# Optimization experiments

Hardware: AMD Instinct MI355X
Metric: run time of the kernel (lower is better)

## Reference

```python
import jax, jax.numpy as jnp
import numpy as np
import math

DIM = 1024
MAX_DEPTH = 16
ROPE_BASE = 10000.0
NUM_ACTIVE = 2

def setup_inputs() -> dict:
    key = jax.random.key(0)
    ks = jax.random.split(key, 6)
    bsz, seq, dim, E, hidden = 4, 1024, DIM, 8, 4 * DIM
    bound = 1.0 / math.sqrt(dim)
    return {
        "x": jax.random.normal(ks[0], (bsz, seq, dim), jnp.float32),
        "router_w": jax.random.normal(ks[1], (dim, dim), jnp.float32) * 0.02,
        "expert_keys": jax.random.uniform(ks[2], (E, dim), jnp.float32, -bound, bound),
        "expert_bias": jnp.zeros((E,), jnp.float32),
        "fc_w": jax.random.normal(ks[3], (E, hidden, dim), jnp.float32) * 0.02,
        "proj_w": jax.random.normal(ks[4], (E, dim, hidden), jnp.float32) * 0.02,
        "depth_idx": 3,
    }

def _rope_row(depth_idx, rev_idx, dtype):
    half = DIM // 2
    inv_freq = 1.0 / (ROPE_BASE ** (jnp.arange(0, DIM, 2, dtype=jnp.float32) / DIM))  # [half]
    f = depth_idx * inv_freq
    r = rev_idx * inv_freq
    return (jnp.cos(f).astype(dtype), jnp.sin(f).astype(dtype),
            jnp.cos(r).astype(dtype), jnp.sin(r).astype(dtype))

def reference(x, router_w, expert_keys, expert_bias, fc_w, proj_w, depth_idx):
    bsz, seq, dim = x.shape
    N = bsz * seq
    flat_x = x.reshape(N, dim)
    # router + RMSNorm (no weight, eps = machine eps, matching F.rms_norm default)
    q = flat_x @ router_w.T
    eps = jnp.asarray(jnp.finfo(q.dtype).eps, q.dtype)
    q = q * jax.lax.rsqrt(jnp.mean(q * q, axis=-1, keepdims=True) + eps)
    # depth RoPE (forward freq on first half pairing, reverse freq on second half)
    half = dim // 2
    cos, sin, rcos, rsin = _rope_row(float(depth_idx), float(MAX_DEPTH - 1 - depth_idx), q.dtype)
    q1, q2 = q[..., :half], q[..., half:]
    q = jnp.concatenate((q1 * cos + q2 * sin, -q1 * rsin + q2 * rcos), axis=-1)
    # routing
    logits = (q @ expert_keys.T) / math.sqrt(dim)  # [N, E]
    gate_values = jax.nn.sigmoid(logits)
    biased = logits + expert_bias
    _, topk_idx = jax.lax.top_k(biased, NUM_ACTIVE)  # [N, k]
    topk_gates = jnp.take_along_axis(gate_values, topk_idx, axis=-1)
    topk_gates = topk_gates / jnp.clip(topk_gates.sum(-1, keepdims=True), 1e-9, None)
    gates = jnp.zeros_like(gate_values).at[jnp.arange(N)[:, None], topk_idx].set(topk_gates)
    # dense all-expert MLP: relu(x W_fc^T)^2 W_proj^T, then mask-and-sum
    h = jax.nn.relu(jnp.einsum('nd,ehd->neh', flat_x, fc_w))
    expert_out = jnp.einsum('neh,edh->ned', h * h, proj_w)  # [N, E, dim]
    y = jnp.einsum('ned,ne->nd', expert_out, gates)
    return y.reshape(bsz, seq, dim)
```

## Files before the change

kernel.cpp:

```cpp
#include <hip/hip_runtime.h>
#include <hip/hip_bf16.h>
#include <math.h>

#define N_TOK 4096
#define DIM_V 1024
#define NEXP  8
#define HID   4096
#define NSLOT 9216

typedef short  s16x8 __attribute__((ext_vector_type(8)));
typedef unsigned short u16x8 __attribute__((ext_vector_type(8)));
typedef float  f32x4 __attribute__((ext_vector_type(4)));

constexpr size_t OFF_XB   = 0;
constexpr size_t OFF_WB   = OFF_XB + 8388608;
constexpr size_t OFF_RK   = OFF_WB + 2097152;
constexpr size_t OFF_KPP  = OFF_RK + 65536;
constexpr size_t OFF_SSQ  = OFF_KPP + 65536;
constexpr size_t OFF_CNT  = OFF_SSQ + 16384;
constexpr size_t OFF_CUR  = OFF_CNT + 128;
constexpr size_t OFF_TOK  = OFF_CUR + 128;
constexpr size_t OFF_GSL  = OFF_TOK + 36864;
constexpr size_t ZERO_BEG = OFF_KPP;
constexpr size_t ZERO_END = OFF_GSL + 36864;
constexpr size_t OFF_OFFP = ZERO_END;
constexpr size_t OFF_IDX2 = OFF_OFFP + 128;
constexpr size_t OFF_G2   = OFF_IDX2 + 32768;
constexpr size_t OFF_INV  = OFF_G2 + 32768;
constexpr size_t SMALL_END = OFF_INV + 32768;

constexpr size_t A_OFF_FCB = SMALL_END;
constexpr size_t A_OFF_PO  = A_OFF_FCB;
constexpr size_t A_OFF_PJB = A_OFF_FCB + 67108864;
constexpr size_t A_OFF_H2  = A_OFF_PJB + 67108864;
constexpr size_t WS_FULL   = A_OFF_H2 + 75497472;

__device__ inline unsigned short f2bf(float f) {
  __hip_bfloat16 h = __float2bfloat16(f);
  return __builtin_bit_cast(unsigned short, h);
}

__device__ __forceinline__ void gload16(const void* g, void* l) {
  __builtin_amdgcn_global_load_lds(
      (const __attribute__((address_space(1))) unsigned int*)g,
      (__attribute__((address_space(3))) unsigned int*)l, 16, 0, 0);
}

__global__ __launch_bounds__(256) void k_cvt_all(
    const float* __restrict__ x, const float* __restrict__ rw,
    const float* __restrict__ fw, const float* __restrict__ pw,
    unsigned short* __restrict__ xb, unsigned short* __restrict__ wb,
    unsigned short* __restrict__ fcb, unsigned short* __restrict__ pjb) {
  constexpr int NX4 = (N_TOK * DIM_V) / 4;
  constexpr int NW4 = (DIM_V * DIM_V) / 4;
  constexpr int NF4 = (NEXP * HID * DIM_V) / 4;
  constexpr int NU  = (NX4 + NW4 + 2 * NF4) / 1024;
  const int upb = (NU + (int)gridDim.x - 1) / (int)gridDim.x;
  for (int k = 0; k < upb; ++k) {
    int u = (int)blockIdx.x * upb + k;
    if (u >= NU) break;
    int f4 = u * 1024;
    const float4* s; unsigned short* d; int base;
    if (f4 < NX4)                   { s = (const float4*)x;  d = xb;  base = f4; }
    else if (f4 < NX4 + NW4)        { s = (const float4*)rw; d = wb;  base = f4 - NX4; }
    else if (f4 < NX4 + NW4 + NF4)  { s = (const float4*)fw; d = fcb; base = f4 - NX4 - NW4; }
    else                            { s = (const float4*)pw; d = pjb; base = f4 - NX4 - NW4 - NF4; }
    int j = base + (int)threadIdx.x;
    float4 v0 = s[j];
    float4 v1 = s[j + 256];
    float4 v2 = s[j + 512];
    float4 v3 = s[j + 768];
    ushort4 o0 = { f2bf(v0.x), f2bf(v0.y), f2bf(v0.z), f2bf(v0.w) };
    ushort4 o1 = { f2bf(v1.x), f2bf(v1.y), f2bf(v1.z), f2bf(v1.w) };
    ushort4 o2 = { f2bf(v2.x), f2bf(v2.y), f2bf(v2.z), f2bf(v2.w) };
    ushort4 o3 = { f2bf(v3.x), f2bf(v3.y), f2bf(v3.z), f2bf(v3.w) };
    *(ushort4*)(d + (size_t)j * 4)           = o0;
    *(ushort4*)(d + (size_t)(j + 256) * 4)   = o1;
    *(ushort4*)(d + (size_t)(j + 512) * 4)   = o2;
    *(ushort4*)(d + (size_t)(j + 768) * 4)   = o3;
  }
}

__global__ void k_ropekeys(const float* __restrict__ keys, const int* __restrict__ depth,
                           double* __restrict__ rk) {
  int i = threadIdx.x;
  if (i >= 512) return;
  int dep = depth[0];
  double p = pow(10000.0, (double)i / 512.0);
  float invf = 1.0f / (float)p;
  float ff = (float)dep * invf;
  float rr = (float)(15 - dep) * invf;
  float cf  = (float)cos((double)ff);
  float sf  = (float)sin((double)ff);
  float rcf = (float)cos((double)rr);
  float rsf = (float)sin((double)rr);
  for (int e = 0; e < NEXP; ++e) {
    double k1 = (double)keys[e * DIM_V + i];
    double k2 = (double)keys[e * DIM_V + 512 + i];
    rk[e * DIM_V + i]       = (double)cf  * k1 - (double)rsf * k2;
    rk[e * DIM_V + 512 + i] = (double)sf  * k1 + (double)rcf * k2;
  }
}

__global__ __launch_bounds__(256) void k_colsum(const float* __restrict__ W,
                                                const double* __restrict__ rk,
                                                double* __restrict__ kpp) {
  int j  = blockIdx.x * 256 + threadIdx.x;
  int d0 = blockIdx.y * 64;
  double acc[NEXP] = {};
  for (int dd = 0; dd < 64; ++dd) {
    int d = d0 + dd;
    double w = (double)W[(size_t)d * DIM_V + j];
#pragma unroll
    for (int e = 0; e < NEXP; ++e) acc[e] += w * rk[e * DIM_V + d];
  }
  for (int e = 0; e < NEXP; ++e) atomicAdd(&kpp[e * DIM_V + j], acc[e]);
}

__global__ __launch_bounds__(256) void k_gate(const float* __restrict__ x,
                                              const double* __restrict__ kpp,
                                              const float* __restrict__ sumsq,
                                              const float* __restrict__ bias,
                                              int* __restrict__ idx2, float* __restrict__ gates2,
                                              int* __restrict__ counts) {
  int wave = (blockIdx.x * 256 + threadIdx.x) >> 6;
  int lane = threadIdx.x & 63;
  if (wave >= N_TOK) return;
  const float4* xr = (const float4*)(x + (size_t)wave * DIM_V);
  double a[NEXP] = {};
#pragma unroll
  for (int j = 0; j < 4; ++j) {
    int c = lane + 64 * j;
    float4 v = xr[c];
#pragma unroll
    for (int e = 0; e < NEXP; ++e) {
      const double* kp = kpp + (size_t)e * DIM_V + c * 4;
      a[e] += (double)v.x * kp[0] + (double)v.y * kp[1] +
              (double)v.z * kp[2] + (double)v.w * kp[3];
    }
  }
#pragma unroll
  for (int e = 0; e < NEXP; ++e)
    for (int d = 1; d < 64; d <<= 1) a[e] += __shfl_xor(a[e], d, 64);
  if (lane == 0) {
    float s = rsqrtf(sumsq[wave] * (1.0f / 1024.0f) + 1.1920928955078125e-7f);
    float z[NEXP], b[NEXP];
#pragma unroll
    for (int e = 0; e < NEXP; ++e) {
      z[e] = (float)(a[e] * (double)s * (1.0 / 32.0));
      b[e] = z[e] + bias[e];
    }
    int i1 = 0;
    for (int e = 1; e < NEXP; ++e) if (b[e] > b[i1]) i1 = e;
    int i2 = -1;
    for (int e = 0; e < NEXP; ++e) if (e != i1 && (i2 < 0 || b[e] > b[i2])) i2 = e;
    float g1 = 1.f / (1.f + expf(-z[i1]));
    float g2 = 1.f / (1.f + expf(-z[i2]));
    float sm = fmaxf(g1 + g2, 1e-9f);
    idx2[wave * 2] = i1; idx2[wave * 2 + 1] = i2;
    gates2[wave * 2] = g1 / sm; gates2[wave * 2 + 1] = g2 / sm;
    atomicAdd(&counts[i1], 1); atomicAdd(&counts[i2], 1);
  }
}

__global__ void k_scatter(const int* __restrict__ idx2, const float* __restrict__ gates2,
                          const int* __restrict__ counts, int* __restrict__ cursor,
                          int* __restrict__ tok, float* __restrict__ gsl,
                          int* __restrict__ inv, int* __restrict__ offp_out) {
  int off[NEXP + 1];
  off[0] = 0;
  for (int e = 0; e < NEXP; ++e) off[e + 1] = off[e] + ((counts[e] + 127) & ~127);
  int n = blockIdx.x * 256 + threadIdx.x;
  if (blockIdx.x == 0 && threadIdx.x == 0)
    for (int e = 0; e <= NEXP; ++e) offp_out[e] = off[e];
  if (n >= N_TOK) return;
  for (int r = 0; r < 2; ++r) {
    int e = idx2[n * 2 + r];
    int pos = atomicAdd(&cursor[e], 1);
    int slot = off[e] + pos;
    tok[slot] = n; gsl[slot] = gates2[n * 2 + r]; inv[n * 2 + r] = slot;
  }
}

__global__ __launch_bounds__(512) void k_fc256(
    const unsigned short* __restrict__ xb,
    const unsigned short* __restrict__ fcb,
    const int* __restrict__ offp, const int* __restrict__ tok,
    unsigned short* __restrict__ h2) {
  constexpr int KD = DIM_V;
  constexpr int NT = KD / 64;
  const int G = gridDim.x, q = G >> 3;
  const int idp = ((int)blockIdx.x & 7) * q + ((int)blockIdx.x >> 3);
  const int bx = idp >> 4;
  const int n0 = (idp & 15) * 256;
  int c = 0, e = 0, m0 = -1;
  for (e = 0; e < NEXP; ++e) {
    int nb = (offp[e + 1] - offp[e] + 255) >> 8;
    if (bx < c + nb) { m0 = offp[e] + (bx - c) * 256; break; }
    c += nb;
  }
  if (m0 < 0) return;
  const int segend = offp[e + 1];
  const unsigned short* Bp = fcb + ((size_t)e * HID + n0) * KD;

  __shared__ alignas(16) char smem[131072];
  const int tid = threadIdx.x, wid = tid >> 6, lane = tid & 63;
  const int wr = (wid >> 2) * 128, wcc = (wid & 3) * 64;
  const int swc8 = ((tid & 7) ^ ((tid >> 3) & 7)) * 8;
  const int frow = lane & 15, fsl = lane >> 4, fkey = lane & 7;

  int arow[4];
#pragma unroll
  for (int p = 0; p < 4; ++p) {
    int rr = m0 + p * 64 + (tid >> 3);
    arow[p] = tok[rr < NSLOT ? rr : NSLOT - 1];
  }

  auto stage = [&](int k0s, unsigned db) {
#pragma unroll
    for (int p = 0; p < 4; ++p)
      gload16(xb + (size_t)arow[p] * KD + k0s + swc8,
              smem + db + p * 8192 + wid * 1024);
#pragma unroll
    for (int p = 0; p < 4; ++p)
      gload16(Bp + (size_t)(p * 64 + (tid >> 3)) * KD + k0s + swc8,
              smem + db + 32768 + p * 8192 + wid * 1024);
  };

  f32x4 acc[8][4] = {};
  stage(0, 0);
  for (int t = 0; t < NT; ++t) {
    int tn = t + 1; if (tn == NT) tn = 0;
    stage(tn * 64, (unsigned)((t + 1) & 1) * 65536u);
    asm volatile("s_waitcnt vmcnt(8)" ::: "memory");
    __builtin_amdgcn_s_barrier();
    __builtin_amdgcn_sched_barrier(0);
    const unsigned Ab = (unsigned)(t & 1) * 65536u, Bb = Ab + 32768u;
#pragma unroll
    for (int kk2 = 0; kk2 < 2; ++kk2) {
      const unsigned so = (unsigned)(((fsl + kk2 * 4) ^ fkey) << 4);
      s16x8 af[8], bfr[4];
#pragma unroll
      for (int m = 0; m < 8; ++m)
        af[m] = *(const s16x8*)(smem + Ab + (unsigned)(wr + m * 16 + frow) * 128 + so);
#pragma unroll
      for (int n = 0; n < 4; ++n)
        bfr[n] = *(const s16x8*)(smem + Bb + (unsigned)(wcc + n * 16 + frow) * 128 + so);
      __builtin_amdgcn_s_setprio(1);
#pragma unroll
      for (int m = 0; m < 8; ++m)
#pragma unroll
        for (int n = 0; n < 4; ++n)
          acc[m][n] = __builtin_amdgcn_mfma_f32_16x16x32_bf16(af[m], bfr[n], acc[m][n], 0, 0, 0);
      __builtin_amdgcn_s_setprio(0);
    }
    __builtin_amdgcn_sched_barrier(0);
    __builtin_amdgcn_s_barrier();
  }
#pragma unroll
  for (int m = 0; m < 8; ++m)
#pragma unroll
    for (int j = 0; j < 4; ++j) {
      const int grow = m0 + wr + m * 16 + (lane >> 4) * 4 + j;
      if (grow < segend) {
#pragma unroll
        for (int n = 0; n < 4; ++n) {
          float v = acc[m][n][j];
          v = v > 0.f ? v * v : 0.f;
          h2[(size_t)grow * HID + n0 + wcc + n * 16 + (lane & 15)] = f2bf(v);
        }
      }
    }
}

template<int KD, int ONB, int EPI>
__global__ __launch_bounds__(256) void k_gemm(
    const unsigned short* __restrict__ Aptr,
    const unsigned short* __restrict__ Wptr,
    const int* __restrict__ offp,
    const float* __restrict__ gsl, void* __restrict__ outp) {
  constexpr int GNB = ONB / 128;
  constexpr int NT  = KD / 64;
  const int G = gridDim.x, q = G >> 3;
  const int idp = ((int)blockIdx.x & 7) * q + ((int)blockIdx.x >> 3);
  const int n0 = (idp % GNB) * 128, m0 = (idp / GNB) * 128;
  int e = 0;
  if constexpr (EPI == 1) {
    if (m0 >= offp[NEXP]) return;
    while (e < NEXP - 1 && m0 >= offp[e + 1]) ++e;
  }
  const unsigned short* Bp = Wptr + ((size_t)e * ONB + n0) * KD;

  __shared__ alignas(16) char smem[65536];
  const int tid = threadIdx.x, wid = tid >> 6, lane = tid & 63;
  const int wr = (wid >> 1) * 64, wc = (wid & 1) * 64;
  const int rql  = tid >> 3;
  const int swc8 = ((tid & 7) ^ ((tid >> 3) & 7)) * 8;
  const int frow = lane & 15, fsl = lane >> 4, fkey = lane & 7;

  auto stage = [&](int k0s, unsigned db) {
#pragma unroll
    for (int p = 0; p < 4; ++p)
      gload16(Aptr + (size_t)(m0 + p * 32 + rql) * KD + k0s + swc8,
              smem + db + p * 4096 + wid * 1024);
#pragma unroll
    for (int p = 0; p < 4; ++p)
      gload16(Bp + (size_t)(p * 32 + rql) * KD + k0s + swc8,
              smem + db + 16384 + p * 4096 + wid * 1024);
  };

  f32x4 acc[4][4] = {};
  stage(0, 0);
#pragma unroll 2
  for (int t = 0; t < NT; ++t) {
    int tn = t + 1; if (tn == NT) tn = 0;
    stage(tn * 64, (unsigned)((t + 1) & 1) * 32768u);
    asm volatile("s_waitcnt vmcnt(8)" ::: "memory");
    __builtin_amdgcn_s_barrier();
    __builtin_amdgcn_sched_barrier(0);
    const unsigned Ab = (unsigned)(t & 1) * 32768u, Bb = Ab + 16384u;
    s16x8 af[2][4], bfr[2][4];
#pragma unroll
    for (int kk2 = 0; kk2 < 2; ++kk2) {
      const unsigned so = (unsigned)(((fsl + kk2 * 4) ^ fkey) << 4);
#pragma unroll
      for (int m = 0; m < 4; ++m)
        af[kk2][m] = *(const s16x8*)(smem + Ab + (unsigned)(wr + m * 16 + frow) * 128 + so);
#pragma unroll
      for (int n = 0; n < 4; ++n)
        bfr[kk2][n] = *(const s16x8*)(smem + Bb + (unsigned)(wc + n * 16 + frow) * 128 + so);
    }
    __builtin_amdgcn_s_setprio(1);
#pragma unroll
    for (int kk2 = 0; kk2 < 2; ++kk2)
#pragma unroll
      for (int m = 0; m < 4; ++m)
#pragma unroll
        for (int n = 0; n < 4; ++n)
          acc[m][n] = __builtin_amdgcn_mfma_f32_16x16x32_bf16(af[kk2][m], bfr[kk2][n],
                                                              acc[m][n], 0, 0, 0);
    __builtin_amdgcn_s_setprio(0);
    __builtin_amdgcn_sched_barrier(0);
    __builtin_amdgcn_s_barrier();
  }

#pragma unroll
  for (int m = 0; m < 4; ++m)
#pragma unroll
    for (int j = 0; j < 4; ++j) {
      const int grow = m0 + wr + m * 16 + (lane >> 4) * 4 + j;
      if constexpr (EPI == 0) {
        float s = 0.f;
#pragma unroll
        for (int n = 0; n < 4; ++n) { float v = acc[m][n][j]; s += v * v; }
        s += __shfl_xor(s, 1, 64); s += __shfl_xor(s, 2, 64);
        s += __shfl_xor(s, 4, 64); s += __shfl_xor(s, 8, 64);
        if ((lane & 15) == 0) atomicAdd(&((float*)outp)[grow], s);
      } else {
        float* out = (float*)outp;
        const float g = gsl[grow];
#pragma unroll
        for (int n = 0; n < 4; ++n)
          out[(size_t)grow * ONB + n0 + wc + n * 16 + (lane & 15)] = acc[m][n][j] * g;
      }
    }
}

__global__ void k_combine(const float* __restrict__ po, const int* __restrict__ inv,
                          float* __restrict__ y) {
  const int total = N_TOK * (DIM_V / 4);
  for (int i = blockIdx.x * blockDim.x + threadIdx.x; i < total;
       i += gridDim.x * blockDim.x) {
    int n = i >> 8, c = i & 255;
    int s1 = inv[n * 2], s2 = inv[n * 2 + 1];
    float4 a = ((const float4*)(po + (size_t)s1 * DIM_V))[c];
    float4 b = ((const float4*)(po + (size_t)s2 * DIM_V))[c];
    float4 o; o.x = a.x + b.x; o.y = a.y + b.y; o.z = a.z + b.z; o.w = a.w + b.w;
    ((float4*)(y + (size_t)n * DIM_V))[c] = o;
  }
}

extern "C" void kernel_launch(void* const* d_in, const int* in_sizes, int n_in,
                              void* d_out, int out_size, void* d_ws, size_t ws_size,
                              hipStream_t stream) {
  if (ws_size < WS_FULL) return;
  const float* x      = (const float*)d_in[0];
  const float* rw     = (const float*)d_in[1];
  const float* keys   = (const float*)d_in[2];
  const float* bias   = (const float*)d_in[3];
  const float* fc_w   = (const float*)d_in[4];
  const float* proj_w = (const float*)d_in[5];
  const int*   depth  = (const int*)d_in[6];
  char* ws = (char*)d_ws;
  unsigned short* xb  = (unsigned short*)(ws + OFF_XB);
  unsigned short* wb  = (unsigned short*)(ws + OFF_WB);
  double* rk    = (double*)(ws + OFF_RK);
  double* kpp   = (double*)(ws + OFF_KPP);
  float*  ssq   = (float*)(ws + OFF_SSQ);
  int*    cnt   = (int*)(ws + OFF_CNT);
  int*    cur   = (int*)(ws + OFF_CUR);
  int*    tok   = (int*)(ws + OFF_TOK);
  float*  gsl   = (float*)(ws + OFF_GSL);
  int*    offp  = (int*)(ws + OFF_OFFP);
  int*    idx2  = (int*)(ws + OFF_IDX2);
  float*  g2    = (float*)(ws + OFF_G2);
  int*    inv   = (int*)(ws + OFF_INV);
  unsigned short* fcb = (unsigned short*)(ws + A_OFF_FCB);
  unsigned short* pjb = (unsigned short*)(ws + A_OFF_PJB);
  unsigned short* h2  = (unsigned short*)(ws + A_OFF_H2);
  float*  po    = (float*)(ws + A_OFF_PO);
  float*  y     = (float*)d_out;

  hipMemsetAsync(ws + ZERO_BEG, 0, ZERO_END - ZERO_BEG, stream);
  k_cvt_all<<<2048, 256, 0, stream>>>(x, rw, fc_w, proj_w, xb, wb, fcb, pjb);
  k_ropekeys<<<1, 512, 0, stream>>>(keys, depth, rk);
  k_colsum<<<dim3(4, 16), 256, 0, stream>>>(rw, rk, kpp);
  k_gemm<DIM_V, DIM_V, 0><<<dim3(32 * 8), 256, 0, stream>>>(xb, wb, offp, gsl, ssq);
  k_gate<<<1024, 256, 0, stream>>>(x, kpp, ssq, bias, idx2, g2, cnt);
  k_scatter<<<16, 256, 0, stream>>>(idx2, g2, cnt, cur, tok, gsl, inv, offp);
  k_fc256<<<dim3(44 * 16), 512, 0, stream>>>(xb, fcb, offp, tok, h2);
  k_gemm<HID, DIM_V, 1><<<dim3(72 * 8), 256, 0, stream>>>(h2, pjb, offp, gsl, po);
  k_combine<<<2048, 256, 0, stream>>>(po, inv, y);
}
```

Before: 474.5 us.

## Split gemm template into single-buffered proj kernel and add nontemporal conversion

```diff
diff --git a/kernel.cpp b/kernel.cpp
--- a/kernel.cpp
+++ b/kernel.cpp
@@ -10,6 +10,7 @@
 
 typedef short  s16x8 __attribute__((ext_vector_type(8)));
 typedef unsigned short u16x8 __attribute__((ext_vector_type(8)));
+typedef unsigned short u16x4 __attribute__((ext_vector_type(4)));
 typedef float  f32x4 __attribute__((ext_vector_type(4)));
 
 constexpr size_t OFF_XB   = 0;
@@ -66,18 +67,19 @@
     else if (f4 < NX4 + NW4 + NF4)  { s = (const float4*)fw; d = fcb; base = f4 - NX4 - NW4; }
     else                            { s = (const float4*)pw; d = pjb; base = f4 - NX4 - NW4 - NF4; }
     int j = base + (int)threadIdx.x;
-    float4 v0 = s[j];
-    float4 v1 = s[j + 256];
-    float4 v2 = s[j + 512];
-    float4 v3 = s[j + 768];
-    ushort4 o0 = { f2bf(v0.x), f2bf(v0.y), f2bf(v0.z), f2bf(v0.w) };
-    ushort4 o1 = { f2bf(v1.x), f2bf(v1.y), f2bf(v1.z), f2bf(v1.w) };
-    ushort4 o2 = { f2bf(v2.x), f2bf(v2.y), f2bf(v2.z), f2bf(v2.w) };
-    ushort4 o3 = { f2bf(v3.x), f2bf(v3.y), f2bf(v3.z), f2bf(v3.w) };
-    *(ushort4*)(d + (size_t)j * 4)           = o0;
-    *(ushort4*)(d + (size_t)(j + 256) * 4)   = o1;
-    *(ushort4*)(d + (size_t)(j + 512) * 4)   = o2;
-    *(ushort4*)(d + (size_t)(j + 768) * 4)   = o3;
+    const f32x4* s4 = (const f32x4*)s;
+    f32x4 v0 = __builtin_nontemporal_load(s4 + j);
+    f32x4 v1 = __builtin_nontemporal_load(s4 + j + 256);
+    f32x4 v2 = __builtin_nontemporal_load(s4 + j + 512);
+    f32x4 v3 = __builtin_nontemporal_load(s4 + j + 768);
+    u16x4 o0 = { f2bf(v0.x), f2bf(v0.y), f2bf(v0.z), f2bf(v0.w) };
+    u16x4 o1 = { f2bf(v1.x), f2bf(v1.y), f2bf(v1.z), f2bf(v1.w) };
+    u16x4 o2 = { f2bf(v2.x), f2bf(v2.y), f2bf(v2.z), f2bf(v2.w) };
+    u16x4 o3 = { f2bf(v3.x), f2bf(v3.y), f2bf(v3.z), f2bf(v3.w) };
+    __builtin_nontemporal_store(o0, (u16x4*)(d + (size_t)j * 4));
+    __builtin_nontemporal_store(o1, (u16x4*)(d + (size_t)(j + 256) * 4));
+    __builtin_nontemporal_store(o2, (u16x4*)(d + (size_t)(j + 512) * 4));
+    __builtin_nontemporal_store(o3, (u16x4*)(d + (size_t)(j + 768) * 4));
   }
 }
 
@@ -273,23 +275,80 @@
     }
 }
 
-template<int KD, int ONB, int EPI>
-__global__ __launch_bounds__(256) void k_gemm(
-    const unsigned short* __restrict__ Aptr,
-    const unsigned short* __restrict__ Wptr,
-    const int* __restrict__ offp,
-    const float* __restrict__ gsl, void* __restrict__ outp) {
-  constexpr int GNB = ONB / 128;
+__global__ __launch_bounds__(256) void k_proj1b(
+    const unsigned short* __restrict__ h2,
+    const unsigned short* __restrict__ pjb,
+    const int* __restrict__ offp, const float* __restrict__ gsl,
+    float* __restrict__ po) {
+  constexpr int KD = HID;
+  constexpr int GNB = DIM_V / 128;
   constexpr int NT  = KD / 64;
   const int G = gridDim.x, q = G >> 3;
   const int idp = ((int)blockIdx.x & 7) * q + ((int)blockIdx.x >> 3);
   const int n0 = (idp % GNB) * 128, m0 = (idp / GNB) * 128;
-  int e = 0;
-  if constexpr (EPI == 1) {
-    if (m0 >= offp[NEXP]) return;
-    while (e < NEXP - 1 && m0 >= offp[e + 1]) ++e;
-  }
-  const unsigned short* Bp = Wptr + ((size_t)e * ONB + n0) * KD;
+  if (m0 >= offp[NEXP]) return;
+  int e = 0; while (e < NEXP - 1 && m0 >= offp[e + 1]) ++e;
+  const unsigned short* Bp = pjb + ((size_t)e * DIM_V + n0) * KD;
+
+  __shared__ alignas(16) char smem[32768];
+  const int tid = threadIdx.x, wid = tid >> 6, lane = tid & 63;
+  const int wr = (wid >> 1) * 64, wc = (wid & 1) * 64;
+  const int rql  = tid >> 3;
+  const int swc8 = ((tid & 7) ^ ((tid >> 3) & 7)) * 8;
+  const int frow = lane & 15, fsl = lane >> 4, fkey = lane & 7;
+
+  f32x4 acc[4][4] = {};
+  for (int t = 0; t < NT; ++t) {
+    __syncthreads();
+#pragma unroll
+    for (int p = 0; p < 4; ++p)
+      gload16(h2 + (size_t)(m0 + p * 32 + rql) * KD + t * 64 + swc8,
+              smem + p * 4096 + wid * 1024);
+#pragma unroll
+    for (int p = 0; p < 4; ++p)
+      gload16(Bp + (size_t)(p * 32 + rql) * KD + t * 64 + swc8,
+              smem + 16384 + p * 4096 + wid * 1024);
+    __syncthreads();
+#pragma unroll
+    for (int kk2 = 0; kk2 < 2; ++kk2) {
+      const unsigned so = (unsigned)(((fsl + kk2 * 4) ^ fkey) << 4);
+      s16x8 af[4], bfr[4];
+#pragma unroll
+      for (int m = 0; m < 4; ++m)
+        af[m] = *(const s16x8*)(smem + (unsigned)(wr + m * 16 + frow) * 128 + so);
+#pragma unroll
+      for (int n = 0; n < 4; ++n)
+        bfr[n] = *(const s16x8*)(smem + 16384u + (unsigned)(wc + n * 16 + frow) * 128 + so);
+#pragma unroll
+      for (int m = 0; m < 4; ++m)
+#pragma unroll
+        for (int n = 0; n < 4; ++n)
+          acc[m][n] = __builtin_amdgcn_mfma_f32_16x16x32_bf16(af[m], bfr[n], acc[m][n], 0, 0, 0);
+    }
+  }
+#pragma unroll
+  for (int m = 0; m < 4; ++m)
+#pragma unroll
+    for (int j = 0; j < 4; ++j) {
+      const int grow = m0 + wr + m * 16 + (lane >> 4) * 4 + j;
+      const float g = gsl[grow];
+#pragma unroll
+      for (int n = 0; n < 4; ++n)
+        po[(size_t)grow * DIM_V + n0 + wc + n * 16 + (lane & 15)] = acc[m][n][j] * g;
+    }
+}
+
+__global__ __launch_bounds__(256) void k_qt(
+    const unsigned short* __restrict__ Aptr,
+    const unsigned short* __restrict__ Wptr,
+    float* __restrict__ sumsq) {
+  constexpr int KD = DIM_V;
+  constexpr int GNB = DIM_V / 128;
+  constexpr int NT  = KD / 64;
+  const int G = gridDim.x, q = G >> 3;
+  const int idp = ((int)blockIdx.x & 7) * q + ((int)blockIdx.x >> 3);
+  const int n0 = (idp % GNB) * 128, m0 = (idp / GNB) * 128;
+  const unsigned short* Bp = Wptr + (size_t)n0 * KD;
 
   __shared__ alignas(16) char smem[65536];
   const int tid = threadIdx.x, wid = tid >> 6, lane = tid & 63;
@@ -349,20 +408,12 @@
 #pragma unroll
     for (int j = 0; j < 4; ++j) {
       const int grow = m0 + wr + m * 16 + (lane >> 4) * 4 + j;
-      if constexpr (EPI == 0) {
-        float s = 0.f;
-#pragma unroll
-        for (int n = 0; n < 4; ++n) { float v = acc[m][n][j]; s += v * v; }
-        s += __shfl_xor(s, 1, 64); s += __shfl_xor(s, 2, 64);
-        s += __shfl_xor(s, 4, 64); s += __shfl_xor(s, 8, 64);
-        if ((lane & 15) == 0) atomicAdd(&((float*)outp)[grow], s);
-      } else {
-        float* out = (float*)outp;
-        const float g = gsl[grow];
-#pragma unroll
-        for (int n = 0; n < 4; ++n)
-          out[(size_t)grow * ONB + n0 + wc + n * 16 + (lane & 15)] = acc[m][n][j] * g;
-      }
+      float s = 0.f;
+#pragma unroll
+      for (int n = 0; n < 4; ++n) { float v = acc[m][n][j]; s += v * v; }
+      s += __shfl_xor(s, 1, 64); s += __shfl_xor(s, 2, 64);
+      s += __shfl_xor(s, 4, 64); s += __shfl_xor(s, 8, 64);
+      if ((lane & 15) == 0) atomicAdd(&sumsq[grow], s);
     }
 }
 
@@ -412,13 +463,13 @@
   float*  y     = (float*)d_out;
 
   hipMemsetAsync(ws + ZERO_BEG, 0, ZERO_END - ZERO_BEG, stream);
-  k_cvt_all<<<2048, 256, 0, stream>>>(x, rw, fc_w, proj_w, xb, wb, fcb, pjb);
+  k_cvt_all<<<2208, 256, 0, stream>>>(x, rw, fc_w, proj_w, xb, wb, fcb, pjb);
   k_ropekeys<<<1, 512, 0, stream>>>(keys, depth, rk);
   k_colsum<<<dim3(4, 16), 256, 0, stream>>>(rw, rk, kpp);
-  k_gemm<DIM_V, DIM_V, 0><<<dim3(32 * 8), 256, 0, stream>>>(xb, wb, offp, gsl, ssq);
+  k_qt<<<dim3(32 * 8), 256, 0, stream>>>(xb, wb, ssq);
   k_gate<<<1024, 256, 0, stream>>>(x, kpp, ssq, bias, idx2, g2, cnt);
   k_scatter<<<16, 256, 0, stream>>>(idx2, g2, cnt, cur, tok, gsl, inv, offp);
   k_fc256<<<dim3(44 * 16), 512, 0, stream>>>(xb, fcb, offp, tok, h2);
-  k_gemm<HID, DIM_V, 1><<<dim3(72 * 8), 256, 0, stream>>>(h2, pjb, offp, gsl, po);
+  k_proj1b<<<dim3(72 * 8), 256, 0, stream>>>(h2, pjb, offp, gsl, po);
   k_combine<<<2048, 256, 0, stream>>>(po, inv, y);
 }
```

New measurement: 527.0 us. 11.1% more time.
